# Performance work log

Measured on AMD Instinct MI355X. Metric: run time of the kernel, lower is better.

The kernel has to match this reference:

```python
import jax, jax.numpy as jnp
import numpy as np

N = 8192      # nodes
E = 524288    # edges
F_IN = 256
H = 2         # heads
F_OUT = 128   # per-head out channels
LN_EPS = 1e-5
NEG_SLOPE = 0.2


def setup_inputs() -> dict:
    key = jax.random.key(0)
    ks = jax.random.split(key, 12)
    s = 0.05
    inp = {
        "x": jax.random.normal(ks[0], (N, F_IN), jnp.float32),
        "edge_index": jax.random.randint(ks[1], (2, E), 0, N, jnp.int32),
        "W_gat": jax.random.normal(ks[2], (F_IN, H * F_OUT), jnp.float32) * s,
        "att_src": jax.random.normal(ks[3], (H, F_OUT), jnp.float32) * s,
        "att_dst": jax.random.normal(ks[4], (H, F_OUT), jnp.float32) * s,
        "bias_gat": jnp.zeros((H * F_OUT,), jnp.float32),
        "w_a": jax.random.normal(ks[5], (256, 128), jnp.float32) * s,
        "b_a": jnp.zeros((128,), jnp.float32),
        "g_a": jnp.ones((128,), jnp.float32),
        "be_a": jnp.zeros((128,), jnp.float32),
        "w1": jax.random.normal(ks[6], (128, 64), jnp.float32) * s,
        "b1": jnp.zeros((64,), jnp.float32),
        "g1": jnp.ones((64,), jnp.float32),
        "be1": jnp.zeros((64,), jnp.float32),
        "w2": jax.random.normal(ks[7], (64, 32), jnp.float32) * s,
        "b2": jnp.zeros((32,), jnp.float32),
        "g2": jnp.ones((32,), jnp.float32),
        "be2": jnp.zeros((32,), jnp.float32),
        "w3": jax.random.normal(ks[8], (32, 3), jnp.float32) * s,
        "b3": jnp.zeros((3,), jnp.float32),
    }
    return inp


def _layernorm(x, g, b):
    mu = jnp.mean(x, axis=-1, keepdims=True)
    var = jnp.mean(jnp.square(x - mu), axis=-1, keepdims=True)
    return (x - mu) * jax.lax.rsqrt(var + LN_EPS) * g + b


def _gat_conv(x, edge_index, W, a_src, a_dst, bias):
    # PyG GATConv with add_self_loops=True, concat=True, dropout=0
    loop = jnp.arange(N, dtype=edge_index.dtype)
    src = jnp.concatenate([edge_index[0], loop])  # [E+N]
    dst = jnp.concatenate([edge_index[1], loop])
    h = (x @ W).reshape(N, H, F_OUT)              # per-node transform
    a_s = jnp.sum(h * a_src, axis=-1)             # [N,H]
    a_d = jnp.sum(h * a_dst, axis=-1)             # [N,H]
    e = jax.nn.leaky_relu(a_s[src] + a_d[dst], NEG_SLOPE)  # [E+N,H]
    # segment softmax over incoming edges of each dst node
    emax = jax.ops.segment_max(e, dst, num_segments=N)
    ex = jnp.exp(e - emax[dst])
    denom = jax.ops.segment_sum(ex, dst, num_segments=N)
    alpha = ex / (denom[dst] + 1e-16)             # [E+N,H]
    msg = h[src] * alpha[:, :, None]              # [E+N,H,F_OUT]
    out = jax.ops.segment_sum(msg, dst, num_segments=N)
    return out.reshape(N, H * F_OUT) + bias


def _safe_cdist(z):
    sq = jnp.sum(z * z, axis=-1)                  # [N]
    d2 = sq[:, None] + sq[None, :] - 2.0 * (z @ z.T)
    d2 = jnp.maximum(d2, 0.0)
    pos = d2 > 0
    return jnp.where(pos, jnp.sqrt(jnp.where(pos, d2, 1.0)), 0.0)


def reference(x, edge_index, W_gat, att_src, att_dst, bias_gat,
              w_a, b_a, g_a, be_a, w1, b1, g1, be1,
              w2, b2, g2, be2, w3, b3):
    h = _gat_conv(x, edge_index, W_gat, att_src, att_dst, bias_gat)
    h = jax.nn.relu(h)
    h = jax.nn.relu(_layernorm(h @ w_a + b_a, g_a, be_a))
    h = jax.nn.relu(_layernorm(h @ w1 + b1, g1, be1))
    h = jax.nn.relu(_layernorm(h @ w2 + b2, g2, be2))
    h = h @ w3 + b3                               # [N,3]
    return _safe_cdist(h)                         # [N,N]
```

## Files before the change

kernel.cpp:

```cpp
#include <hip/hip_runtime.h>
#include <hip/hip_bf16.h>

#define N_NODES 8192
#define E_EDGES 524288
#define F_IN    256
#define NH      2
#define F_OUT   128
#define C0      256

__global__ __launch_bounds__(256) void gemm_xw_k(const float* __restrict__ A,
                                                 const float* __restrict__ B,
                                                 float* __restrict__ C) {
  const int K = 256, NC = 256;
  __shared__ float As[16][65];
  __shared__ float Bs[16][65];
  int bm = blockIdx.y * 64;
  int bn = blockIdx.x * 64;
  int tid = threadIdx.x;
  int tm = (tid >> 4) << 2;
  int tn = (tid & 15) << 2;
  float acc[4][4] = {};
  for (int k0 = 0; k0 < K; k0 += 16) {
#pragma unroll
    for (int i = 0; i < 4; i++) {
      int idx = tid + i * 256;
      int m = idx >> 4, k = idx & 15;
      As[k][m] = A[(bm + m) * K + k0 + k];
    }
#pragma unroll
    for (int i = 0; i < 4; i++) {
      int idx = tid + i * 256;
      int k = idx >> 6, n = idx & 63;
      Bs[k][n] = B[(k0 + k) * NC + bn + n];
    }
    __syncthreads();
#pragma unroll
    for (int k = 0; k < 16; k++) {
      float a0 = As[k][tm], a1 = As[k][tm + 1], a2 = As[k][tm + 2], a3 = As[k][tm + 3];
      float b0 = Bs[k][tn], b1 = Bs[k][tn + 1], b2 = Bs[k][tn + 2], b3 = Bs[k][tn + 3];
      acc[0][0] += a0 * b0; acc[0][1] += a0 * b1; acc[0][2] += a0 * b2; acc[0][3] += a0 * b3;
      acc[1][0] += a1 * b0; acc[1][1] += a1 * b1; acc[1][2] += a1 * b2; acc[1][3] += a1 * b3;
      acc[2][0] += a2 * b0; acc[2][1] += a2 * b1; acc[2][2] += a2 * b2; acc[2][3] += a2 * b3;
      acc[3][0] += a3 * b0; acc[3][1] += a3 * b1; acc[3][2] += a3 * b2; acc[3][3] += a3 * b3;
    }
    __syncthreads();
  }
#pragma unroll
  for (int i = 0; i < 4; i++)
#pragma unroll
    for (int j = 0; j < 4; j++)
      C[(bm + tm + i) * NC + bn + tn + j] = acc[i][j];
}

__global__ __launch_bounds__(256) void att_scores_k(const float* __restrict__ h,
                                                    const float* __restrict__ att_src,
                                                    const float* __restrict__ att_dst,
                                                    float* __restrict__ a_s,
                                                    float* __restrict__ a_d) {
  int wave = threadIdx.x >> 6;
  int lane = threadIdx.x & 63;
  int node = blockIdx.x * 4 + wave;
  if (node >= N_NODES) return;
  const float* row = h + (size_t)node * C0;
  float s0 = 0, d0 = 0, s1 = 0, d1 = 0;
  for (int i = lane; i < F_OUT; i += 64) {
    float v0 = row[i], v1 = row[F_OUT + i];
    s0 += v0 * att_src[i];          d0 += v0 * att_dst[i];
    s1 += v1 * att_src[F_OUT + i];  d1 += v1 * att_dst[F_OUT + i];
  }
#pragma unroll
  for (int off = 32; off; off >>= 1) {
    s0 += __shfl_down(s0, off); d0 += __shfl_down(d0, off);
    s1 += __shfl_down(s1, off); d1 += __shfl_down(d1, off);
  }
  if (lane == 0) {
    a_s[node * 2] = s0;     a_d[node * 2] = d0;
    a_s[node * 2 + 1] = s1; a_d[node * 2 + 1] = d1;
  }
}

__global__ __launch_bounds__(256) void hist_k(const int* __restrict__ ei,
                                              int* __restrict__ deg) {
  int e = blockIdx.x * 256 + threadIdx.x;
  if (e < E_EDGES) atomicAdd(&deg[ei[E_EDGES + e]], 1);
}

__global__ __launch_bounds__(256) void scan_k(const int* __restrict__ deg,
                                              int* __restrict__ offs,
                                              int* __restrict__ cursor) {
  __shared__ int sums[256];
  int t = threadIdx.x;
  int local[32];
  int s = 0;
#pragma unroll
  for (int i = 0; i < 32; i++) { local[i] = s; s += deg[t * 32 + i]; }
  sums[t] = s;
  __syncthreads();
  for (int off = 1; off < 256; off <<= 1) {
    int u = (t >= off) ? sums[t - off] : 0;
    __syncthreads();
    if (t >= off) sums[t] += u;
    __syncthreads();
  }
  int base = sums[t] - s;
#pragma unroll
  for (int i = 0; i < 32; i++) {
    int o = base + local[i];
    offs[t * 32 + i] = o;
    cursor[t * 32 + i] = o;
  }
  if (t == 255) offs[N_NODES] = sums[255];
}

__global__ __launch_bounds__(256) void scatter_src_k(const int* __restrict__ ei,
                                                     int* __restrict__ cursor,
                                                     int* __restrict__ sorted_src) {
  int e = blockIdx.x * 256 + threadIdx.x;
  if (e < E_EDGES) {
    int d = ei[E_EDGES + e];
    int p = atomicAdd(&cursor[d], 1);
    sorted_src[p] = ei[e];
  }
}

__global__ __launch_bounds__(256) void gat_gather_k(const int* __restrict__ sorted_src,
                                                    const int* __restrict__ offs,
                                                    const float* __restrict__ h,
                                                    const float* __restrict__ a_s,
                                                    const float* __restrict__ a_d,
                                                    float* __restrict__ gat) {
  int wave = threadIdx.x >> 6;
  int lane = threadIdx.x & 63;
  int node = blockIdx.x * 4 + wave;
  if (node >= N_NODES) return;
  int start = offs[node], end = offs[node + 1];
  float ad0 = a_d[node * 2], ad1 = a_d[node * 2 + 1];
  int head = lane >> 5;
  float4 acc = {0, 0, 0, 0};
  float den0 = 0, den1 = 0;
  for (int base = start; base < end; base += 64) {
    int idx = base + lane;
    int s = -1;
    float e0 = 0, e1 = 0;
    if (idx < end) {
      s = sorted_src[idx];
      float v0 = a_s[s * 2] + ad0;     v0 = v0 > 0.0f ? v0 : 0.2f * v0;
      float v1 = a_s[s * 2 + 1] + ad1; v1 = v1 > 0.0f ? v1 : 0.2f * v1;
      e0 = __expf(v0);
      e1 = __expf(v1);
      den0 += e0; den1 += e1;
    }
    int cnt = min(64, end - base);
    for (int j = 0; j < cnt; j++) {
      int sj = __shfl(s, j);
      float x0 = __shfl(e0, j);
      float x1 = __shfl(e1, j);
      float exh = head ? x1 : x0;
      const float4 hv = *(const float4*)(h + (size_t)sj * C0 + lane * 4);
      acc.x += hv.x * exh; acc.y += hv.y * exh;
      acc.z += hv.z * exh; acc.w += hv.w * exh;
    }
  }
  {
    float v0 = a_s[node * 2] + ad0;     v0 = v0 > 0.0f ? v0 : 0.2f * v0;
    float v1 = a_s[node * 2 + 1] + ad1; v1 = v1 > 0.0f ? v1 : 0.2f * v1;
    float e0 = __expf(v0), e1 = __expf(v1);
    if (lane == 0) { den0 += e0; den1 += e1; }
    float exh = head ? e1 : e0;
    const float4 hv = *(const float4*)(h + (size_t)node * C0 + lane * 4);
    acc.x += hv.x * exh; acc.y += hv.y * exh;
    acc.z += hv.z * exh; acc.w += hv.w * exh;
  }
#pragma unroll
  for (int off = 32; off; off >>= 1) {
    den0 += __shfl_xor(den0, off);
    den1 += __shfl_xor(den1, off);
  }
  float denh = head ? den1 : den0;
  float inv = 1.0f / (denh + 1e-16f);
  float4 o = {acc.x * inv, acc.y * inv, acc.z * inv, acc.w * inv};
  *(float4*)(gat + (size_t)node * C0 + lane * 4) = o;
}

template <int KDIM, int ODIM, bool APPLY_IN>
__global__ __launch_bounds__(256) void fused_layer_k(const float* __restrict__ in,
                                                     const float* __restrict__ bias_in,
                                                     const float* __restrict__ W,
                                                     const float* __restrict__ b,
                                                     const float* __restrict__ g,
                                                     const float* __restrict__ be,
                                                     float* __restrict__ out) {
  const int TILE = 16;
  const int GROUPS = 256 / ODIM;
  const int NPT = TILE / GROUPS;
  __shared__ float in_t[TILE][KDIM + 1];
  __shared__ float out_t[TILE][ODIM + 1];
  int tid = threadIdx.x;
  int n0 = blockIdx.x * TILE;
  for (int idx = tid; idx < TILE * KDIM; idx += 256) {
    int n = idx / KDIM, k = idx % KDIM;
    float v = in[(size_t)(n0 + n) * KDIM + k];
    if (APPLY_IN) v = fmaxf(v + bias_in[k], 0.0f);
    in_t[n][k] = v;
  }
  __syncthreads();
  int jj = tid % ODIM;
  int grp = tid / ODIM;
  float acc[NPT];
#pragma unroll
  for (int t = 0; t < NPT; t++) acc[t] = b[jj];
  for (int k = 0; k < KDIM; k++) {
    float w = W[k * ODIM + jj];
#pragma unroll
    for (int t = 0; t < NPT; t++) acc[t] += in_t[grp + t * GROUPS][k] * w;
  }
#pragma unroll
  for (int t = 0; t < NPT; t++) out_t[grp + t * GROUPS][jj] = acc[t];
  __syncthreads();
  const int TPN = 256 / TILE;
  const int JPT = ODIM / TPN;
  int node = tid / TPN;
  int ln = tid % TPN;
  float v[JPT];
  float s = 0;
#pragma unroll
  for (int q = 0; q < JPT; q++) { v[q] = out_t[node][ln + q * TPN]; s += v[q]; }
#pragma unroll
  for (int m = 1; m < TPN; m <<= 1) s += __shfl_xor(s, m);
  float mu = s / (float)ODIM;
  float vs = 0;
#pragma unroll
  for (int q = 0; q < JPT; q++) { float dd = v[q] - mu; vs += dd * dd; }
#pragma unroll
  for (int m = 1; m < TPN; m <<= 1) vs += __shfl_xor(vs, m);
  float inv = rsqrtf(vs / (float)ODIM + 1e-5f);
#pragma unroll
  for (int q = 0; q < JPT; q++) {
    int j = ln + q * TPN;
    float o = (v[q] - mu) * inv * g[j] + be[j];
    out[(size_t)(n0 + node) * ODIM + j] = fmaxf(o, 0.0f);
  }
}

__global__ __launch_bounds__(256) void final_z_k(const float* __restrict__ h2,
                                                 const float* __restrict__ w3,
                                                 const float* __restrict__ b3,
                                                 float* __restrict__ z) {
  int n = blockIdx.x * 256 + threadIdx.x;
  if (n >= N_NODES) return;
  float a0 = b3[0], a1 = b3[1], a2 = b3[2];
  const float* row = h2 + (size_t)n * 32;
#pragma unroll
  for (int k = 0; k < 32; k++) {
    float v = row[k];
    a0 += v * w3[k * 3 + 0];
    a1 += v * w3[k * 3 + 1];
    a2 += v * w3[k * 3 + 2];
  }
  float4 zz = {a0, a1, a2, 0.0f};
  ((float4*)z)[n] = zz;
}

__global__ __launch_bounds__(256) void cdist_k(const float* __restrict__ z,
                                               float* __restrict__ out) {
  int i = blockIdx.x >> 3;
  int j0 = (((blockIdx.x & 7) << 8) + threadIdx.x) << 2;
  const float4 zi = ((const float4*)z)[i];
  float4 r;
  {
    float4 zj = ((const float4*)z)[j0 + 0];
    float dx = zi.x - zj.x, dy = zi.y - zj.y, dz = zi.z - zj.z;
    r.x = sqrtf(dx * dx + dy * dy + dz * dz);
  }
  {
    float4 zj = ((const float4*)z)[j0 + 1];
    float dx = zi.x - zj.x, dy = zi.y - zj.y, dz = zi.z - zj.z;
    r.y = sqrtf(dx * dx + dy * dy + dz * dz);
  }
  {
    float4 zj = ((const float4*)z)[j0 + 2];
    float dx = zi.x - zj.x, dy = zi.y - zj.y, dz = zi.z - zj.z;
    r.z = sqrtf(dx * dx + dy * dy + dz * dz);
  }
  {
    float4 zj = ((const float4*)z)[j0 + 3];
    float dx = zi.x - zj.x, dy = zi.y - zj.y, dz = zi.z - zj.z;
    r.w = sqrtf(dx * dx + dy * dy + dz * dz);
  }
  ((float4*)out)[((size_t)i * N_NODES + j0) >> 2] = r;
}

extern "C" void kernel_launch(void* const* d_in, const int* in_sizes, int n_in,
                              void* d_out, int out_size, void* d_ws, size_t ws_size,
                              hipStream_t stream) {
  const float* x        = (const float*)d_in[0];
  const int*   ei       = (const int*)d_in[1];
  const float* W_gat    = (const float*)d_in[2];
  const float* att_src  = (const float*)d_in[3];
  const float* att_dst  = (const float*)d_in[4];
  const float* bias_gat = (const float*)d_in[5];
  const float* w_a      = (const float*)d_in[6];
  const float* b_a      = (const float*)d_in[7];
  const float* g_a      = (const float*)d_in[8];
  const float* be_a     = (const float*)d_in[9];
  const float* w1       = (const float*)d_in[10];
  const float* b1       = (const float*)d_in[11];
  const float* g1       = (const float*)d_in[12];
  const float* be1      = (const float*)d_in[13];
  const float* w2       = (const float*)d_in[14];
  const float* b2       = (const float*)d_in[15];
  const float* g2       = (const float*)d_in[16];
  const float* be2      = (const float*)d_in[17];
  const float* w3       = (const float*)d_in[18];
  const float* b3       = (const float*)d_in[19];
  float* out = (float*)d_out;

  float* ws = (float*)d_ws;
  float* h     = ws;
  float* a_s   = h + 2097152;
  float* a_d   = a_s + 16384;
  float* gat   = a_d + 16384;
  float* hA    = gat + 2097152;
  float* h1    = hA + 1048576;
  float* h2    = h1 + 524288;
  float* z     = h2 + 262144;
  int*   deg    = (int*)(z + 32768);
  int*   offs   = deg + 8192;
  int*   cursor = offs + 8200;
  int*   sorted = cursor + 8192;

  hipMemsetAsync(deg, 0, N_NODES * sizeof(int), stream);

  gemm_xw_k<<<dim3(4, 128), 256, 0, stream>>>(x, W_gat, h);
  att_scores_k<<<2048, 256, 0, stream>>>(h, att_src, att_dst, a_s, a_d);
  hist_k<<<E_EDGES / 256, 256, 0, stream>>>(ei, deg);
  scan_k<<<1, 256, 0, stream>>>(deg, offs, cursor);
  scatter_src_k<<<E_EDGES / 256, 256, 0, stream>>>(ei, cursor, sorted);
  gat_gather_k<<<2048, 256, 0, stream>>>(sorted, offs, h, a_s, a_d, gat);
  fused_layer_k<256, 128, true><<<N_NODES / 16, 256, 0, stream>>>(gat, bias_gat, w_a, b_a, g_a, be_a, hA);
  fused_layer_k<128, 64, false><<<N_NODES / 16, 256, 0, stream>>>(hA, nullptr, w1, b1, g1, be1, h1);
  fused_layer_k<64, 32, false><<<N_NODES / 16, 256, 0, stream>>>(h1, nullptr, w2, b2, g2, be2, h2);
  final_z_k<<<N_NODES / 256, 256, 0, stream>>>(h2, w3, b3, z);
  cdist_k<<<N_NODES * 8, 256, 0, stream>>>(z, out);
}
```

Baseline: 523.1 us.

## Vectorize loads across kernels and use nontemporal stores for cdist output

Switches shared and global accesses in the GEMM, attention-score, gather, fused-layer and final projection kernels to float4/float2 loads and stores, with padding adjusted for alignment. The gather inner loop is unrolled by two so two neighbour rows are in flight at once. The large NxN distance output now uses nontemporal stores to avoid polluting cache. The main intended win is the 256MB cdist write; padding changes may add LDS bank conflicts.

After: 484.8 us. 7.3% less time.

```diff
diff --git a/kernel.cpp b/kernel.cpp
--- a/kernel.cpp
+++ b/kernel.cpp
@@ -8,12 +8,14 @@
 #define F_OUT   128
 #define C0      256
 
+typedef float f32x4 __attribute__((ext_vector_type(4)));
+
 __global__ __launch_bounds__(256) void gemm_xw_k(const float* __restrict__ A,
                                                  const float* __restrict__ B,
                                                  float* __restrict__ C) {
   const int K = 256, NC = 256;
-  __shared__ float As[16][65];
-  __shared__ float Bs[16][65];
+  __shared__ float As[16][68];
+  __shared__ float Bs[16][68];
   int bm = blockIdx.y * 64;
   int bn = blockIdx.x * 64;
   int tid = threadIdx.x;
@@ -36,20 +38,20 @@
     __syncthreads();
 #pragma unroll
     for (int k = 0; k < 16; k++) {
-      float a0 = As[k][tm], a1 = As[k][tm + 1], a2 = As[k][tm + 2], a3 = As[k][tm + 3];
-      float b0 = Bs[k][tn], b1 = Bs[k][tn + 1], b2 = Bs[k][tn + 2], b3 = Bs[k][tn + 3];
-      acc[0][0] += a0 * b0; acc[0][1] += a0 * b1; acc[0][2] += a0 * b2; acc[0][3] += a0 * b3;
-      acc[1][0] += a1 * b0; acc[1][1] += a1 * b1; acc[1][2] += a1 * b2; acc[1][3] += a1 * b3;
-      acc[2][0] += a2 * b0; acc[2][1] += a2 * b1; acc[2][2] += a2 * b2; acc[2][3] += a2 * b3;
-      acc[3][0] += a3 * b0; acc[3][1] += a3 * b1; acc[3][2] += a3 * b2; acc[3][3] += a3 * b3;
+      float4 a = *(const float4*)&As[k][tm];
+      float4 b = *(const float4*)&Bs[k][tn];
+      acc[0][0] += a.x * b.x; acc[0][1] += a.x * b.y; acc[0][2] += a.x * b.z; acc[0][3] += a.x * b.w;
+      acc[1][0] += a.y * b.x; acc[1][1] += a.y * b.y; acc[1][2] += a.y * b.z; acc[1][3] += a.y * b.w;
+      acc[2][0] += a.z * b.x; acc[2][1] += a.z * b.y; acc[2][2] += a.z * b.z; acc[2][3] += a.z * b.w;
+      acc[3][0] += a.w * b.x; acc[3][1] += a.w * b.y; acc[3][2] += a.w * b.z; acc[3][3] += a.w * b.w;
     }
     __syncthreads();
   }
 #pragma unroll
-  for (int i = 0; i < 4; i++)
-#pragma unroll
-    for (int j = 0; j < 4; j++)
-      C[(bm + tm + i) * NC + bn + tn + j] = acc[i][j];
+  for (int i = 0; i < 4; i++) {
+    float4 o = {acc[i][0], acc[i][1], acc[i][2], acc[i][3]};
+    *(float4*)&C[(bm + tm + i) * NC + bn + tn] = o;
+  }
 }
 
 __global__ __launch_bounds__(256) void att_scores_k(const float* __restrict__ h,
@@ -61,22 +63,18 @@
   int lane = threadIdx.x & 63;
   int node = blockIdx.x * 4 + wave;
   if (node >= N_NODES) return;
-  const float* row = h + (size_t)node * C0;
-  float s0 = 0, d0 = 0, s1 = 0, d1 = 0;
-  for (int i = lane; i < F_OUT; i += 64) {
-    float v0 = row[i], v1 = row[F_OUT + i];
-    s0 += v0 * att_src[i];          d0 += v0 * att_dst[i];
-    s1 += v1 * att_src[F_OUT + i];  d1 += v1 * att_dst[F_OUT + i];
-  }
-#pragma unroll
-  for (int off = 32; off; off >>= 1) {
-    s0 += __shfl_down(s0, off); d0 += __shfl_down(d0, off);
-    s1 += __shfl_down(s1, off); d1 += __shfl_down(d1, off);
-  }
-  if (lane == 0) {
-    a_s[node * 2] = s0;     a_d[node * 2] = d0;
-    a_s[node * 2 + 1] = s1; a_d[node * 2 + 1] = d1;
-  }
+  const float4 hv = *(const float4*)(h + (size_t)node * C0 + lane * 4);
+  const float4 vs = *(const float4*)(att_src + lane * 4);
+  const float4 vd = *(const float4*)(att_dst + lane * 4);
+  float s = hv.x * vs.x + hv.y * vs.y + hv.z * vs.z + hv.w * vs.w;
+  float d = hv.x * vd.x + hv.y * vd.y + hv.z * vd.z + hv.w * vd.w;
+#pragma unroll
+  for (int off = 16; off; off >>= 1) {
+    s += __shfl_xor(s, off);
+    d += __shfl_xor(d, off);
+  }
+  if (lane == 0)  { a_s[node * 2] = s;     a_d[node * 2] = d; }
+  if (lane == 32) { a_s[node * 2 + 1] = s; a_d[node * 2 + 1] = d; }
 }
 
 __global__ __launch_bounds__(256) void hist_k(const int* __restrict__ ei,
@@ -134,7 +132,8 @@
   int node = blockIdx.x * 4 + wave;
   if (node >= N_NODES) return;
   int start = offs[node], end = offs[node + 1];
-  float ad0 = a_d[node * 2], ad1 = a_d[node * 2 + 1];
+  const float2 adv = *(const float2*)(a_d + node * 2);
+  float ad0 = adv.x, ad1 = adv.y;
   int head = lane >> 5;
   float4 acc = {0, 0, 0, 0};
   float den0 = 0, den1 = 0;
@@ -144,14 +143,28 @@
     float e0 = 0, e1 = 0;
     if (idx < end) {
       s = sorted_src[idx];
-      float v0 = a_s[s * 2] + ad0;     v0 = v0 > 0.0f ? v0 : 0.2f * v0;
-      float v1 = a_s[s * 2 + 1] + ad1; v1 = v1 > 0.0f ? v1 : 0.2f * v1;
+      const float2 asv = *(const float2*)(a_s + s * 2);
+      float v0 = asv.x + ad0; v0 = v0 > 0.0f ? v0 : 0.2f * v0;
+      float v1 = asv.y + ad1; v1 = v1 > 0.0f ? v1 : 0.2f * v1;
       e0 = __expf(v0);
       e1 = __expf(v1);
       den0 += e0; den1 += e1;
     }
     int cnt = min(64, end - base);
-    for (int j = 0; j < cnt; j++) {
+    int j = 0;
+    for (; j + 2 <= cnt; j += 2) {
+      int sj0 = __shfl(s, j);
+      int sj1 = __shfl(s, j + 1);
+      float a00 = __shfl(e0, j),     a10 = __shfl(e1, j);
+      float a01 = __shfl(e0, j + 1), a11 = __shfl(e1, j + 1);
+      const float4 hv0 = *(const float4*)(h + (size_t)sj0 * C0 + lane * 4);
+      const float4 hv1 = *(const float4*)(h + (size_t)sj1 * C0 + lane * 4);
+      float w0 = head ? a10 : a00;
+      float w1 = head ? a11 : a01;
+      acc.x += hv0.x * w0; acc.y += hv0.y * w0; acc.z += hv0.z * w0; acc.w += hv0.w * w0;
+      acc.x += hv1.x * w1; acc.y += hv1.y * w1; acc.z += hv1.z * w1; acc.w += hv1.w * w1;
+    }
+    if (j < cnt) {
       int sj = __shfl(s, j);
       float x0 = __shfl(e0, j);
       float x1 = __shfl(e1, j);
@@ -162,8 +175,9 @@
     }
   }
   {
-    float v0 = a_s[node * 2] + ad0;     v0 = v0 > 0.0f ? v0 : 0.2f * v0;
-    float v1 = a_s[node * 2 + 1] + ad1; v1 = v1 > 0.0f ? v1 : 0.2f * v1;
+    const float2 asv = *(const float2*)(a_s + node * 2);
+    float v0 = asv.x + ad0; v0 = v0 > 0.0f ? v0 : 0.2f * v0;
+    float v1 = asv.y + ad1; v1 = v1 > 0.0f ? v1 : 0.2f * v1;
     float e0 = __expf(v0), e1 = __expf(v1);
     if (lane == 0) { den0 += e0; den1 += e1; }
     float exh = head ? e1 : e0;
@@ -193,15 +207,22 @@
   const int TILE = 16;
   const int GROUPS = 256 / ODIM;
   const int NPT = TILE / GROUPS;
-  __shared__ float in_t[TILE][KDIM + 1];
+  __shared__ float in_t[TILE][KDIM + 4];
   __shared__ float out_t[TILE][ODIM + 1];
   int tid = threadIdx.x;
   int n0 = blockIdx.x * TILE;
-  for (int idx = tid; idx < TILE * KDIM; idx += 256) {
-    int n = idx / KDIM, k = idx % KDIM;
-    float v = in[(size_t)(n0 + n) * KDIM + k];
-    if (APPLY_IN) v = fmaxf(v + bias_in[k], 0.0f);
-    in_t[n][k] = v;
+  const int KD4 = KDIM / 4;
+  for (int idx = tid; idx < TILE * KD4; idx += 256) {
+    int n = idx / KD4, k4 = idx % KD4;
+    float4 v = *(const float4*)&in[(size_t)(n0 + n) * KDIM + k4 * 4];
+    if (APPLY_IN) {
+      const float4 bb = *(const float4*)&bias_in[k4 * 4];
+      v.x = fmaxf(v.x + bb.x, 0.0f);
+      v.y = fmaxf(v.y + bb.y, 0.0f);
+      v.z = fmaxf(v.z + bb.z, 0.0f);
+      v.w = fmaxf(v.w + bb.w, 0.0f);
+    }
+    *(float4*)&in_t[n][k4 * 4] = v;
   }
   __syncthreads();
   int jj = tid % ODIM;
@@ -209,10 +230,16 @@
   float acc[NPT];
 #pragma unroll
   for (int t = 0; t < NPT; t++) acc[t] = b[jj];
-  for (int k = 0; k < KDIM; k++) {
-    float w = W[k * ODIM + jj];
-#pragma unroll
-    for (int t = 0; t < NPT; t++) acc[t] += in_t[grp + t * GROUPS][k] * w;
+  for (int k = 0; k < KDIM; k += 4) {
+    float w0 = W[(k + 0) * ODIM + jj];
+    float w1 = W[(k + 1) * ODIM + jj];
+    float w2 = W[(k + 2) * ODIM + jj];
+    float w3 = W[(k + 3) * ODIM + jj];
+#pragma unroll
+    for (int t = 0; t < NPT; t++) {
+      float4 v = *(const float4*)&in_t[grp + t * GROUPS][k];
+      acc[t] = fmaf(v.w, w3, fmaf(v.z, w2, fmaf(v.y, w1, fmaf(v.x, w0, acc[t]))));
+    }
   }
 #pragma unroll
   for (int t = 0; t < NPT; t++) out_t[grp + t * GROUPS][jj] = acc[t];
@@ -249,13 +276,14 @@
   int n = blockIdx.x * 256 + threadIdx.x;
   if (n >= N_NODES) return;
   float a0 = b3[0], a1 = b3[1], a2 = b3[2];
-  const float* row = h2 + (size_t)n * 32;
-#pragma unroll
-  for (int k = 0; k < 32; k++) {
-    float v = row[k];
-    a0 += v * w3[k * 3 + 0];
-    a1 += v * w3[k * 3 + 1];
-    a2 += v * w3[k * 3 + 2];
+  const float4* row = (const float4*)(h2 + (size_t)n * 32);
+#pragma unroll
+  for (int q = 0; q < 8; q++) {
+    float4 v = row[q];
+    int k = q * 4;
+    a0 += v.x * w3[(k + 0) * 3 + 0] + v.y * w3[(k + 1) * 3 + 0] + v.z * w3[(k + 2) * 3 + 0] + v.w * w3[(k + 3) * 3 + 0];
+    a1 += v.x * w3[(k + 0) * 3 + 1] + v.y * w3[(k + 1) * 3 + 1] + v.z * w3[(k + 2) * 3 + 1] + v.w * w3[(k + 3) * 3 + 1];
+    a2 += v.x * w3[(k + 0) * 3 + 2] + v.y * w3[(k + 1) * 3 + 2] + v.z * w3[(k + 2) * 3 + 2] + v.w * w3[(k + 3) * 3 + 2];
   }
   float4 zz = {a0, a1, a2, 0.0f};
   ((float4*)z)[n] = zz;
@@ -266,7 +294,7 @@
   int i = blockIdx.x >> 3;
   int j0 = (((blockIdx.x & 7) << 8) + threadIdx.x) << 2;
   const float4 zi = ((const float4*)z)[i];
-  float4 r;
+  f32x4 r;
   {
     float4 zj = ((const float4*)z)[j0 + 0];
     float dx = zi.x - zj.x, dy = zi.y - zj.y, dz = zi.z - zj.z;
@@ -287,7 +315,8 @@
     float dx = zi.x - zj.x, dy = zi.y - zj.y, dz = zi.z - zj.z;
     r.w = sqrtf(dx * dx + dy * dy + dz * dz);
   }
-  ((float4*)out)[((size_t)i * N_NODES + j0) >> 2] = r;
+  f32x4* dst = (f32x4*)out + (((size_t)i * N_NODES + j0) >> 2);
+  __builtin_nontemporal_store(r, dst);
 }
 
 extern "C" void kernel_launch(void* const* d_in, const int* in_sizes, int n_in,
```
